# Optimization experiments

Hardware: AMD Instinct MI355X
Metric: run time of the kernel (lower is better)

The kernel has to match this reference:

```python
import jax, jax.numpy as jnp
import numpy as np

N = 100000   # nodes
E = 3200000  # edges (avg degree 32)
F_IN = 767   # Amazon-Computers num_features
H = 16       # hidden (constructor default x=16)
C = 10       # num_classes


def setup_inputs() -> dict:
    key = jax.random.key(0)
    ks = jax.random.split(key, 12)
    def w(k, shape):
        fan_in = shape[0]
        return jax.random.normal(k, shape, jnp.float32) / np.sqrt(fan_in)
    return {
        "x": jax.random.normal(ks[0], (N, F_IN), jnp.float32),
        "edge_index": jax.random.randint(ks[1], (2, E), 0, N, jnp.int32),
        "w1_init": w(ks[2], (F_IN, H)), "w1_root": w(ks[3], (F_IN, H)), "b1": jnp.zeros((H,), jnp.float32),
        "w2_init": w(ks[4], (H, H)),    "w2_root": w(ks[5], (H, H)),    "b2": jnp.zeros((H,), jnp.float32),
        "w3_init": w(ks[6], (H, C)),    "w3_root": w(ks[7], (H, C)),    "b3": jnp.zeros((C,), jnp.float32),
    }


def _gcn_norm(row, col, dtype):
    # PyG ARMAConv: gcn_norm without self-loops: norm_e = deg^{-1/2}[row] * deg^{-1/2}[col]
    deg = jax.ops.segment_sum(jnp.ones((E,), dtype), col, num_segments=N)
    dinv = jnp.where(deg > 0, deg ** -0.5, 0.0)
    return dinv[row] * dinv[col]


def _arma_conv(x, w_init, w_root, b, row, col, norm):
    # K=1 stack, T=1 layer: relu( A_hat @ (x W_init) + x W_root + b )
    h = x @ w_init                                   # [N, F_out]
    msg = h[row] * norm[:, None]                     # [E, F_out] irregular gather
    agg = jax.ops.segment_sum(msg, col, num_segments=N)  # scatter-add to targets
    return jax.nn.relu(agg + x @ w_root + b)


def reference(x, edge_index, w1_init, w1_root, b1, w2_init, w2_root, b2, w3_init, w3_root, b3):
    row, col = edge_index[0], edge_index[1]
    norm = _gcn_norm(row, col, x.dtype)
    # Net.forward (eval mode: dropout = identity). Outer relu after conv1/conv2 is
    # idempotent with ARMAConv's internal relu but kept for faithfulness.
    h = jax.nn.relu(_arma_conv(x, w1_init, w1_root, b1, row, col, norm))
    h = jax.nn.relu(_arma_conv(h, w2_init, w2_root, b2, row, col, norm))
    h = _arma_conv(h, w3_init, w3_root, b3, row, col, norm)
    return jax.nn.log_softmax(h, axis=1)
```

## Files before the change

### kernel.cpp

```cpp
#include <hip/hip_runtime.h>
#include <hip/hip_bf16.h>
#include <cstdint>
#include <cstddef>

#define F_IN 767
#define HD   16


__global__ void k_hist(const int* __restrict__ col, int* __restrict__ cnt, int E) {
  int e = blockIdx.x * 256 + threadIdx.x;
  if (e < E) atomicAdd(&cnt[col[e]], 1);
}

__global__ void k_scan1(const int* __restrict__ cnt, int* __restrict__ off,
                        int* __restrict__ bsum, int N) {
  __shared__ int lds[256];
  int t = threadIdx.x;
  int base = blockIdx.x * 1024 + t * 4;
  int4 v = make_int4(0, 0, 0, 0);
  if (base + 3 < N) {
    v = *(const int4*)&cnt[base];
  } else {
    if (base + 0 < N) v.x = cnt[base + 0];
    if (base + 1 < N) v.y = cnt[base + 1];
    if (base + 2 < N) v.z = cnt[base + 2];
    if (base + 3 < N) v.w = cnt[base + 3];
  }
  int s = v.x + v.y + v.z + v.w;
  lds[t] = s;
  __syncthreads();
  for (int d = 1; d < 256; d <<= 1) {
    int add = (t >= d) ? lds[t - d] : 0;
    __syncthreads();
    lds[t] += add;
    __syncthreads();
  }
  int excl = lds[t] - s;
  if (t == 255) bsum[blockIdx.x] = lds[255];
  int run = excl;
  if (base + 0 < N) off[base + 0] = run; run += v.x;
  if (base + 1 < N) off[base + 1] = run; run += v.y;
  if (base + 2 < N) off[base + 2] = run; run += v.z;
  if (base + 3 < N) off[base + 3] = run;
}

__global__ void k_scan2(int* __restrict__ bsum, int nb) {
  __shared__ int lds[256];
  int t = threadIdx.x;
  int s = (t < nb) ? bsum[t] : 0;
  lds[t] = s;
  __syncthreads();
  for (int d = 1; d < 256; d <<= 1) {
    int add = (t >= d) ? lds[t - d] : 0;
    __syncthreads();
    lds[t] += add;
    __syncthreads();
  }
  if (t < nb) bsum[t] = lds[t] - s;
}

__global__ void k_scan3(const int* __restrict__ cnt, int* __restrict__ off,
                        int* __restrict__ cur, float* __restrict__ dinv,
                        const int* __restrict__ bsum, int N) {
  int i = blockIdx.x * 256 + threadIdx.x;
  if (i < N) {
    int o = off[i] + bsum[i >> 10];
    off[i] = o;
    cur[i] = o;
    int c = cnt[i];
    dinv[i] = (c > 0) ? rsqrtf((float)c) : 0.f;
  }
}

#define PSH     9
#define PA_TILE 4096

__global__ void k_binit(const int* __restrict__ off, int* __restrict__ bcur, int N, int E) {
  int b = threadIdx.x;
  int cb = b << PSH;
  bcur[b] = (cb < N) ? off[cb] : E;
}

__global__ __launch_bounds__(256) void k_part(const int* __restrict__ row,
                                              const int* __restrict__ col,
                                              int* __restrict__ bcur,
                                              int2* __restrict__ tmp, int E) {
  __shared__ int  hcnt[256];
  __shared__ int  hoff[256];
  __shared__ int  hcur[256];
  __shared__ int  gbase[256];
  __shared__ int2 st[PA_TILE];
  int t = threadIdx.x;
  int tile = blockIdx.x * PA_TILE;
  int nE = min(PA_TILE, E - tile);

  hcnt[t] = 0;
  __syncthreads();

  int r[16], c[16];
  #pragma unroll
  for (int i = 0; i < 16; ++i) {
    int li = i * 256 + t;
    if (li < nE) {
      r[i] = row[tile + li];
      c[i] = col[tile + li];
      atomicAdd(&hcnt[c[i] >> PSH], 1);
    } else c[i] = -1;
  }
  __syncthreads();

  int s = hcnt[t];
  hoff[t] = s;
  __syncthreads();
  for (int d = 1; d < 256; d <<= 1) {
    int add = (t >= d) ? hoff[t - d] : 0;
    __syncthreads();
    hoff[t] += add;
    __syncthreads();
  }
  int excl = hoff[t] - s;
  hcur[t] = excl;
  gbase[t] = (s > 0) ? atomicAdd(&bcur[t], s) : 0;
  __syncthreads();

  #pragma unroll
  for (int i = 0; i < 16; ++i) {
    if (c[i] >= 0) {
      int p = atomicAdd(&hcur[c[i] >> PSH], 1);
      st[p] = make_int2(r[i], c[i]);
    }
  }
  __syncthreads();

  #pragma unroll
  for (int i = 0; i < 16; ++i) {
    int idx = i * 256 + t;
    if (idx < nE) {
      int2 v = st[idx];
      int b = v.y >> PSH;
      tmp[gbase[b] + (idx - (hoff[b] - hcnt[b]))] = v;
    }
  }
}

#define PLS 4
__global__ __launch_bounds__(256) void k_place(const int2* __restrict__ tmp,
                                               const int* __restrict__ off,
                                               int* __restrict__ cur,
                                               int* __restrict__ srow, int N, int E) {
  int b = blockIdx.x / PLS, sp = blockIdx.x % PLS;
  int cb = b << PSH;
  if (cb >= N) return;
  int start = off[cb];
  int nx = (b + 1) << PSH;
  int end = (nx < N) ? off[nx] : E;
  int len = end - start;
  int per = (len + PLS - 1) / PLS;
  int s0 = start + sp * per;
  int s1 = min(s0 + per, end);
  for (int e = s0 + threadIdx.x; e < s1; e += 256) {
    int2 v = tmp[e];
    int p = atomicAdd(&cur[v.y], 1);
    srow[p] = v.x;
  }
}

__global__ void k_pack(const float* __restrict__ wi, const float* __restrict__ wr,
                       float* __restrict__ Wc, int K, int H) {
  int i = blockIdx.x * 256 + threadIdx.x;
  int tot = K * 2 * H;
  if (i < tot) {
    int k = i / (2 * H), c = i % (2 * H);
    Wc[i] = (c < H) ? wi[k * H + c] : wr[k * H + (c - H)];
  }
}

#define G1_KC  32
#define G1_M   64

__global__ __launch_bounds__(128) void k_gemm1(const float* __restrict__ x,
                                               const float* __restrict__ Wc,
                                               const float* __restrict__ dinv,
                                               float* __restrict__ T, int N) {
  __shared__ __align__(16) float xs[2][G1_KC * G1_M];
  __shared__ __align__(16) float ws[2][G1_KC * 32];
  int t = threadIdx.x;
  int tn = t & 7;
  int tm = t >> 3;
  int rowBase = blockIdx.x * G1_M;

  int kl = t & 15;
  int rr = t >> 4;
  int sxw = kl & 7;

  float xv[16];
  float wv[8];

  const int NC = (F_IN + G1_KC - 1) / G1_KC;

  float acc[4][4];
  #pragma unroll
  for (int m = 0; m < 4; ++m)
    #pragma unroll
    for (int c = 0; c < 4; ++c) acc[m][c] = 0.f;

  {
    const int kc = 0;
    #pragma unroll
    for (int kh = 0; kh < 2; ++kh) {
      int kg = kc + kh * 16 + kl;
      #pragma unroll
      for (int i = 0; i < 8; ++i) {
        int gr = rowBase + i * 8 + rr;
        float v = 0.f;
        if (gr < N) v = x[(size_t)gr * F_IN + kg];
        xv[i * 2 + kh] = v;
      }
    }
    #pragma unroll
    for (int i = 0; i < 8; ++i) {
      int idx = i * 128 + t;
      int wk = idx >> 5, wc = idx & 31;
      wv[i] = Wc[(size_t)(kc + wk) * 32 + wc];
    }
    #pragma unroll
    for (int kh = 0; kh < 2; ++kh)
      #pragma unroll
      for (int i = 0; i < 8; ++i) {
        int r = i * 8 + rr;
        int q = r >> 2, j = r & 3;
        xs[0][(kh * 16 + kl) * G1_M + ((q ^ sxw) << 2) + j] = xv[i * 2 + kh];
      }
    #pragma unroll
    for (int i = 0; i < 8; ++i) ws[0][i * 128 + t] = wv[i];
  }
  __syncthreads();

  for (int c = 0; c < NC; ++c) {
    int b = c & 1;
    if (c + 1 < NC) {
      int kc = (c + 1) * G1_KC;
      #pragma unroll
      for (int kh = 0; kh < 2; ++kh) {
        int kg = kc + kh * 16 + kl;
        bool kval = (kg < F_IN);
        #pragma unroll
        for (int i = 0; i < 8; ++i) {
          int gr = rowBase + i * 8 + rr;
          float v = 0.f;
          if (kval && gr < N) v = x[(size_t)gr * F_IN + kg];
          xv[i * 2 + kh] = v;
        }
      }
      #pragma unroll
      for (int i = 0; i < 8; ++i) {
        int idx = i * 128 + t;
        int wk = idx >> 5, wc = idx & 31;
        int kg = kc + wk;
        wv[i] = (kg < F_IN) ? Wc[(size_t)kg * 32 + wc] : 0.f;
      }
    }
    const float* xb = &xs[b][0];
    const float* wb = &ws[b][0];
    #pragma unroll
    for (int kk = 0; kk < G1_KC; ++kk) {
      const int s = kk & 7;
      float4 a  = *(const float4*)&xb[kk * G1_M + ((tm ^ s) << 2)];
      float4 bv = *(const float4*)&wb[kk * 32 + tn * 4];
      float am[4] = {a.x, a.y, a.z, a.w};
      float bn[4] = {bv.x, bv.y, bv.z, bv.w};
      #pragma unroll
      for (int m = 0; m < 4; ++m)
        #pragma unroll
        for (int cc = 0; cc < 4; ++cc) acc[m][cc] += am[m] * bn[cc];
    }
    if (c + 1 < NC) {
      __syncthreads();
      #pragma unroll
      for (int kh = 0; kh < 2; ++kh)
        #pragma unroll
        for (int i = 0; i < 8; ++i) {
          int r = i * 8 + rr;
          int q = r >> 2, j = r & 3;
          xs[b ^ 1][(kh * 16 + kl) * G1_M + ((q ^ sxw) << 2) + j] = xv[i * 2 + kh];
        }
      #pragma unroll
      for (int i = 0; i < 8; ++i) ws[b ^ 1][i * 128 + t] = wv[i];
      __syncthreads();
    }
  }

  #pragma unroll
  for (int m = 0; m < 4; ++m) {
    int r = rowBase + tm * 4 + m;
    if (r < N) {
      float4 o = make_float4(acc[m][0], acc[m][1], acc[m][2], acc[m][3]);
      if (tn < 4) {
        float d = dinv[r];
        o.x *= d; o.y *= d; o.z *= d; o.w *= d;
      }
      *(float4*)&T[(size_t)r * 32 + tn * 4] = o;
    }
  }
}

__global__ void k_gemm_small(const float* __restrict__ h, const float* __restrict__ W,
                             const float* __restrict__ dinv,
                             float* __restrict__ T, int N, int P, int SC) {
  int idx = blockIdx.x * 256 + threadIdx.x;
  int n = idx >> 5, c = idx & 31;
  if (n < N && c < P) {
    float acc = 0.f;
    #pragma unroll
    for (int k = 0; k < HD; ++k) acc += h[(size_t)n * HD + k] * W[k * P + c];
    if (c < SC) acc *= dinv[n];
    T[(size_t)n * P + c] = acc;
  }
}

__global__ void k_gather_relu(const float* __restrict__ T, const int* __restrict__ off,
                              const int* __restrict__ cnt, const int* __restrict__ srow,
                              const float* __restrict__ dinv, const float* __restrict__ bias,
                              float* __restrict__ hout, int N) {
  int t = threadIdx.x;
  int j = t & 15, ln = t >> 4;
  int n = blockIdx.x * 16 + ln;
  if (n >= N) return;
  int s = off[n], c = cnt[n];
  float acc = 0.f;
  for (int p = s; p < s + c; ++p) {
    int r = srow[p];
    acc += T[(size_t)r * 32 + j];
  }
  float v = dinv[n] * acc + T[(size_t)n * 32 + 16 + j] + bias[j];
  hout[(size_t)n * HD + j] = fmaxf(v, 0.f);
}

__global__ void k_gather_lsm(const float* __restrict__ T, const int* __restrict__ off,
                             const int* __restrict__ cnt, const int* __restrict__ srow,
                             const float* __restrict__ dinv, const float* __restrict__ b3,
                             float* __restrict__ out, int N) {
  int t = threadIdx.x;
  int j = t & 15, ln = t >> 4;
  int n = blockIdx.x * 16 + ln;
  bool act = (n < N) && (j < 10);
  float v = -1e30f;
  if (act) {
    int s = off[n], c = cnt[n];
    float acc = 0.f;
    for (int p = s; p < s + c; ++p) {
      int r = srow[p];
      acc += T[(size_t)r * 20 + j];
    }
    v = dinv[n] * acc + T[(size_t)n * 20 + 10 + j] + b3[j];
    v = fmaxf(v, 0.f);
  }
  float m = v;
  #pragma unroll
  for (int mask = 8; mask >= 1; mask >>= 1) m = fmaxf(m, __shfl_xor(m, mask, 16));
  float e = act ? __expf(v - m) : 0.f;
  float sum = e;
  #pragma unroll
  for (int mask = 8; mask >= 1; mask >>= 1) sum += __shfl_xor(sum, mask, 16);
  if (act) out[(size_t)n * 10 + j] = (v - m) - __logf(sum);
}

extern "C" void kernel_launch(void* const* d_in, const int* in_sizes, int n_in,
                              void* d_out, int out_size, void* d_ws, size_t ws_size,
                              hipStream_t stream) {
  const float* x    = (const float*)d_in[0];
  const int* eidx   = (const int*)d_in[1];
  const float* w1i  = (const float*)d_in[2];
  const float* w1r  = (const float*)d_in[3];
  const float* b1   = (const float*)d_in[4];
  const float* w2i  = (const float*)d_in[5];
  const float* w2r  = (const float*)d_in[6];
  const float* b2   = (const float*)d_in[7];
  const float* w3i  = (const float*)d_in[8];
  const float* w3r  = (const float*)d_in[9];
  const float* b3   = (const float*)d_in[10];
  float* out = (float*)d_out;

  const int N = in_sizes[0] / F_IN;
  const int E = in_sizes[1] / 2;
  const int* row = eidx;
  const int* col = eidx + E;

  char* p = (char*)d_ws;
  auto alloc = [&](size_t bytes) { void* r = (void*)p; p += (bytes + 255) & ~(size_t)255; return r; };
  int*   cnt  = (int*)alloc((size_t)N * 4);
  int*   off  = (int*)alloc((size_t)N * 4);
  int*   cur  = (int*)alloc((size_t)N * 4);
  float* dinv = (float*)alloc((size_t)N * 4);
  int*   bsum = (int*)alloc(1024);
  int*   bcur = (int*)alloc(1024);
  float* Wc   = (float*)alloc((size_t)F_IN * 32 * 4);
  float* W2c  = (float*)alloc((size_t)HD * 32 * 4);
  float* W3c  = (float*)alloc((size_t)HD * 20 * 4);
  int*   srow = (int*)alloc((size_t)E * 4);
  char*  big  = (char*)alloc((size_t)E * 8);
  int2*  tmp  = (int2*)big;
  float* T    = (float*)big;
  float* h    = (float*)(big + (size_t)N * 32 * 4);

  const int nbE = (E + 255) / 256;
  const int nbScan = (N + 1023) / 1024;
  const int nBuck = (N + (1 << PSH) - 1) >> PSH;

  hipMemsetAsync(cnt, 0, (size_t)N * 4, stream);
  k_hist <<<nbE, 256, 0, stream>>>(col, cnt, E);
  k_scan1<<<nbScan, 256, 0, stream>>>(cnt, off, bsum, N);
  k_scan2<<<1, 256, 0, stream>>>(bsum, nbScan);
  k_scan3<<<(N + 255) / 256, 256, 0, stream>>>(cnt, off, cur, dinv, bsum, N);
  k_binit<<<1, 256, 0, stream>>>(off, bcur, N, E);
  k_part <<<(E + PA_TILE - 1) / PA_TILE, 256, 0, stream>>>(row, col, bcur, tmp, E);
  k_place<<<nBuck * PLS, 256, 0, stream>>>(tmp, off, cur, srow, N, E);

  k_pack<<<(F_IN * 32 + 255) / 256, 256, 0, stream>>>(w1i, w1r, Wc, F_IN, 16);
  k_pack<<<(HD * 32 + 255) / 256, 256, 0, stream>>>(w2i, w2r, W2c, HD, 16);
  k_pack<<<(HD * 20 + 255) / 256, 256, 0, stream>>>(w3i, w3r, W3c, HD, 10);

  k_gemm1<<<(N + G1_M - 1) / G1_M, 128, 0, stream>>>(x, Wc, dinv, T, N);
  k_gather_relu<<<(N + 15) / 16, 256, 0, stream>>>(T, off, cnt, srow, dinv, b1, h, N);
  k_gemm_small<<<(N * 32 + 255) / 256, 256, 0, stream>>>(h, W2c, dinv, T, N, 32, 16);
  k_gather_relu<<<(N + 15) / 16, 256, 0, stream>>>(T, off, cnt, srow, dinv, b2, h, N);
  k_gemm_small<<<(N * 32 + 255) / 256, 256, 0, stream>>>(h, W3c, dinv, T, N, 20, 10);
  k_gather_lsm<<<(N + 15) / 16, 256, 0, stream>>>(T, off, cnt, srow, dinv, b3, out, N);
}
```

Before: 1.095 ms.

## Use bf16 split-precision MFMA for first-layer GEMM and unroll gather loops

New measurement: 934.4 us. 14.6% less time.

```diff
diff --git a/kernel.cpp b/kernel.cpp
--- a/kernel.cpp
+++ b/kernel.cpp
@@ -5,6 +5,18 @@
 
 #define F_IN 767
 #define HD   16
+
+typedef __attribute__((ext_vector_type(8))) short short8v;
+typedef __attribute__((ext_vector_type(4))) float float4v;
+typedef float __attribute__((ext_vector_type(4), aligned(4))) float4a;
+
+static __device__ __forceinline__ unsigned short f2bf(float f) {
+  unsigned int u = __float_as_uint(f);
+  return (unsigned short)((u + 0x7fffu + ((u >> 16) & 1u)) >> 16);
+}
+static __device__ __forceinline__ float bf2f(unsigned short b) {
+  return __uint_as_float(((unsigned int)b) << 16);
+}
 
 
 __global__ void k_hist(const int* __restrict__ col, int* __restrict__ cnt, int E) {
@@ -175,131 +187,81 @@
   }
 }
 
-#define G1_KC  32
-#define G1_M   64
-
-__global__ __launch_bounds__(128) void k_gemm1(const float* __restrict__ x,
-                                               const float* __restrict__ Wc,
+__global__ void k_packbf(const float* __restrict__ wi, const float* __restrict__ wr,
+                         unsigned short* __restrict__ Bf) {
+  int idx = blockIdx.x * 256 + threadIdx.x;
+  if (idx >= 24 * 2 * 2 * 64 * 8) return;
+  int j    = idx & 7;
+  int l    = (idx >> 3) & 63;
+  int half = (idx >> 9) & 1;
+  int term = (idx >> 10) & 1;
+  int s    = idx >> 11;
+  int col  = half * 16 + (l & 15);
+  int k    = s * 32 + (l >> 4) * 8 + j;
+  float w = 0.f;
+  if (k < F_IN) w = (col < 16) ? wi[k * 16 + col] : wr[k * 16 + (col - 16)];
+  unsigned short hi = f2bf(w);
+  unsigned short lo = f2bf(w - bf2f(hi));
+  Bf[idx] = (term == 0) ? hi : lo;
+}
+
+__global__ __launch_bounds__(256) void k_gemm1(const float* __restrict__ x,
+                                               const unsigned short* __restrict__ Bf,
                                                const float* __restrict__ dinv,
                                                float* __restrict__ T, int N) {
-  __shared__ __align__(16) float xs[2][G1_KC * G1_M];
-  __shared__ __align__(16) float ws[2][G1_KC * 32];
-  int t = threadIdx.x;
-  int tn = t & 7;
-  int tm = t >> 3;
-  int rowBase = blockIdx.x * G1_M;
-
-  int kl = t & 15;
-  int rr = t >> 4;
-  int sxw = kl & 7;
-
-  float xv[16];
-  float wv[8];
-
-  const int NC = (F_IN + G1_KC - 1) / G1_KC;
-
-  float acc[4][4];
-  #pragma unroll
-  for (int m = 0; m < 4; ++m)
+  int t = threadIdx.x;
+  int w = t >> 6, l = t & 63;
+  int kg = l >> 4;
+  int rowA = blockIdx.x * 64 + w * 16 + (l & 15);
+  const float* xr = x + (size_t)min(rowA, N - 1) * F_IN;
+  const short8v* Bfv = (const short8v*)Bf;
+
+  float4v c0 = {0.f, 0.f, 0.f, 0.f};
+  float4v c1 = {0.f, 0.f, 0.f, 0.f};
+
+  for (int s = 0; s < 24; ++s) {
+    int kbase = s * 32 + kg * 8;
+    float v[8];
+    if (s < 23) {
+      float4a a = *(const float4a*)(xr + kbase);
+      float4a b = *(const float4a*)(xr + kbase + 4);
+      v[0] = a.x; v[1] = a.y; v[2] = a.z; v[3] = a.w;
+      v[4] = b.x; v[5] = b.y; v[6] = b.z; v[7] = b.w;
+    } else {
+      #pragma unroll
+      for (int j = 0; j < 8; ++j) {
+        int k = kbase + j;
+        v[j] = (k < F_IN) ? xr[k] : 0.f;
+      }
+    }
+    short8v ah, al;
     #pragma unroll
-    for (int c = 0; c < 4; ++c) acc[m][c] = 0.f;
-
-  {
-    const int kc = 0;
-    #pragma unroll
-    for (int kh = 0; kh < 2; ++kh) {
-      int kg = kc + kh * 16 + kl;
-      #pragma unroll
-      for (int i = 0; i < 8; ++i) {
-        int gr = rowBase + i * 8 + rr;
-        float v = 0.f;
-        if (gr < N) v = x[(size_t)gr * F_IN + kg];
-        xv[i * 2 + kh] = v;
-      }
-    }
-    #pragma unroll
-    for (int i = 0; i < 8; ++i) {
-      int idx = i * 128 + t;
-      int wk = idx >> 5, wc = idx & 31;
-      wv[i] = Wc[(size_t)(kc + wk) * 32 + wc];
-    }
-    #pragma unroll
-    for (int kh = 0; kh < 2; ++kh)
-      #pragma unroll
-      for (int i = 0; i < 8; ++i) {
-        int r = i * 8 + rr;
-        int q = r >> 2, j = r & 3;
-        xs[0][(kh * 16 + kl) * G1_M + ((q ^ sxw) << 2) + j] = xv[i * 2 + kh];
-      }
-    #pragma unroll
-    for (int i = 0; i < 8; ++i) ws[0][i * 128 + t] = wv[i];
-  }
-  __syncthreads();
-
-  for (int c = 0; c < NC; ++c) {
-    int b = c & 1;
-    if (c + 1 < NC) {
-      int kc = (c + 1) * G1_KC;
-      #pragma unroll
-      for (int kh = 0; kh < 2; ++kh) {
-        int kg = kc + kh * 16 + kl;
-        bool kval = (kg < F_IN);
-        #pragma unroll
-        for (int i = 0; i < 8; ++i) {
-          int gr = rowBase + i * 8 + rr;
-          float v = 0.f;
-          if (kval && gr < N) v = x[(size_t)gr * F_IN + kg];
-          xv[i * 2 + kh] = v;
-        }
-      }
-      #pragma unroll
-      for (int i = 0; i < 8; ++i) {
-        int idx = i * 128 + t;
-        int wk = idx >> 5, wc = idx & 31;
-        int kg = kc + wk;
-        wv[i] = (kg < F_IN) ? Wc[(size_t)kg * 32 + wc] : 0.f;
-      }
-    }
-    const float* xb = &xs[b][0];
-    const float* wb = &ws[b][0];
-    #pragma unroll
-    for (int kk = 0; kk < G1_KC; ++kk) {
-      const int s = kk & 7;
-      float4 a  = *(const float4*)&xb[kk * G1_M + ((tm ^ s) << 2)];
-      float4 bv = *(const float4*)&wb[kk * 32 + tn * 4];
-      float am[4] = {a.x, a.y, a.z, a.w};
-      float bn[4] = {bv.x, bv.y, bv.z, bv.w};
-      #pragma unroll
-      for (int m = 0; m < 4; ++m)
-        #pragma unroll
-        for (int cc = 0; cc < 4; ++cc) acc[m][cc] += am[m] * bn[cc];
-    }
-    if (c + 1 < NC) {
-      __syncthreads();
-      #pragma unroll
-      for (int kh = 0; kh < 2; ++kh)
-        #pragma unroll
-        for (int i = 0; i < 8; ++i) {
-          int r = i * 8 + rr;
-          int q = r >> 2, j = r & 3;
-          xs[b ^ 1][(kh * 16 + kl) * G1_M + ((q ^ sxw) << 2) + j] = xv[i * 2 + kh];
-        }
-      #pragma unroll
-      for (int i = 0; i < 8; ++i) ws[b ^ 1][i * 128 + t] = wv[i];
-      __syncthreads();
-    }
-  }
-
-  #pragma unroll
-  for (int m = 0; m < 4; ++m) {
-    int r = rowBase + tm * 4 + m;
-    if (r < N) {
-      float4 o = make_float4(acc[m][0], acc[m][1], acc[m][2], acc[m][3]);
-      if (tn < 4) {
-        float d = dinv[r];
-        o.x *= d; o.y *= d; o.z *= d; o.w *= d;
-      }
-      *(float4*)&T[(size_t)r * 32 + tn * 4] = o;
+    for (int j = 0; j < 8; ++j) {
+      unsigned short h = f2bf(v[j]);
+      ah[j] = (short)h;
+      al[j] = (short)f2bf(v[j] - bf2f(h));
+    }
+    short8v bh0 = Bfv[(s * 4 + 0) * 64 + l];
+    short8v bh1 = Bfv[(s * 4 + 1) * 64 + l];
+    short8v bl0 = Bfv[(s * 4 + 2) * 64 + l];
+    short8v bl1 = Bfv[(s * 4 + 3) * 64 + l];
+    c0 = __builtin_amdgcn_mfma_f32_16x16x32_bf16(ah, bh0, c0, 0, 0, 0);
+    c1 = __builtin_amdgcn_mfma_f32_16x16x32_bf16(ah, bh1, c1, 0, 0, 0);
+    c0 = __builtin_amdgcn_mfma_f32_16x16x32_bf16(al, bh0, c0, 0, 0, 0);
+    c1 = __builtin_amdgcn_mfma_f32_16x16x32_bf16(al, bh1, c1, 0, 0, 0);
+    c0 = __builtin_amdgcn_mfma_f32_16x16x32_bf16(ah, bl0, c0, 0, 0, 0);
+    c1 = __builtin_amdgcn_mfma_f32_16x16x32_bf16(ah, bl1, c1, 0, 0, 0);
+  }
+
+  int rowC = blockIdx.x * 64 + w * 16 + (l >> 4) * 4;
+  int colC = l & 15;
+  #pragma unroll
+  for (int j = 0; j < 4; ++j) {
+    int gr = rowC + j;
+    if (gr < N) {
+      float d = dinv[gr];
+      T[(size_t)gr * 32 + colC]      = c0[j] * d;
+      T[(size_t)gr * 32 + 16 + colC] = c1[j];
     }
   }
 }
@@ -328,10 +290,16 @@
   if (n >= N) return;
   int s = off[n], c = cnt[n];
   float acc = 0.f;
-  for (int p = s; p < s + c; ++p) {
-    int r = srow[p];
-    acc += T[(size_t)r * 32 + j];
-  }
+  int p = s, e4 = s + (c & ~3);
+  for (; p < e4; p += 4) {
+    int r0 = srow[p], r1 = srow[p + 1], r2 = srow[p + 2], r3 = srow[p + 3];
+    float v0 = T[(size_t)r0 * 32 + j];
+    float v1 = T[(size_t)r1 * 32 + j];
+    float v2 = T[(size_t)r2 * 32 + j];
+    float v3 = T[(size_t)r3 * 32 + j];
+    acc += v0; acc += v1; acc += v2; acc += v3;
+  }
+  for (; p < s + c; ++p) acc += T[(size_t)srow[p] * 32 + j];
   float v = dinv[n] * acc + T[(size_t)n * 32 + 16 + j] + bias[j];
   hout[(size_t)n * HD + j] = fmaxf(v, 0.f);
 }
@@ -348,10 +316,16 @@
   if (act) {
     int s = off[n], c = cnt[n];
     float acc = 0.f;
-    for (int p = s; p < s + c; ++p) {
-      int r = srow[p];
-      acc += T[(size_t)r * 20 + j];
-    }
+    int p = s, e4 = s + (c & ~3);
+    for (; p < e4; p += 4) {
+      int r0 = srow[p], r1 = srow[p + 1], r2 = srow[p + 2], r3 = srow[p + 3];
+      float v0 = T[(size_t)r0 * 20 + j];
+      float v1 = T[(size_t)r1 * 20 + j];
+      float v2 = T[(size_t)r2 * 20 + j];
+      float v3 = T[(size_t)r3 * 20 + j];
+      acc += v0; acc += v1; acc += v2; acc += v3;
+    }
+    for (; p < s + c; ++p) acc += T[(size_t)srow[p] * 20 + j];
     v = dinv[n] * acc + T[(size_t)n * 20 + 10 + j] + b3[j];
     v = fmaxf(v, 0.f);
   }
@@ -394,7 +368,7 @@
   float* dinv = (float*)alloc((size_t)N * 4);
   int*   bsum = (int*)alloc(1024);
   int*   bcur = (int*)alloc(1024);
-  float* Wc   = (float*)alloc((size_t)F_IN * 32 * 4);
+  unsigned short* Bf = (unsigned short*)alloc((size_t)24 * 2 * 2 * 64 * 8 * 2);
   float* W2c  = (float*)alloc((size_t)HD * 32 * 4);
   float* W3c  = (float*)alloc((size_t)HD * 20 * 4);
   int*   srow = (int*)alloc((size_t)E * 4);
@@ -416,11 +390,11 @@
   k_part <<<(E + PA_TILE - 1) / PA_TILE, 256, 0, stream>>>(row, col, bcur, tmp, E);
   k_place<<<nBuck * PLS, 256, 0, stream>>>(tmp, off, cur, srow, N, E);
 
-  k_pack<<<(F_IN * 32 + 255) / 256, 256, 0, stream>>>(w1i, w1r, Wc, F_IN, 16);
+  k_packbf<<<192, 256, 0, stream>>>(w1i, w1r, Bf);
   k_pack<<<(HD * 32 + 255) / 256, 256, 0, stream>>>(w2i, w2r, W2c, HD, 16);
   k_pack<<<(HD * 20 + 255) / 256, 256, 0, stream>>>(w3i, w3r, W3c, HD, 10);
 
-  k_gemm1<<<(N + G1_M - 1) / G1_M, 128, 0, stream>>>(x, Wc, dinv, T, N);
+  k_gemm1<<<(N + 63) / 64, 256, 0, stream>>>(x, Bf, dinv, T, N);
   k_gather_relu<<<(N + 15) / 16, 256, 0, stream>>>(T, off, cnt, srow, dinv, b1, h, N);
   k_gemm_small<<<(N * 32 + 255) / 256, 256, 0, stream>>>(h, W2c, dinv, T, N, 32, 16);
   k_gather_relu<<<(N + 15) / 16, 256, 0, stream>>>(T, off, cnt, srow, dinv, b2, h, N);
```
